# Kernel tuning notes

Hardware: AMD Instinct MI355X
Metric: run time of the kernel (lower is better)

The kernel has to match this reference:

```python
import jax, jax.numpy as jnp
import numpy as np

N = 1000        # genomes
S = 32          # samples
M = 2_000_000   # total genes
K = 100_000     # sequences (contigs)


def setup_inputs() -> dict:
    key = jax.random.key(0)
    k1, k2, k3, k4, k5 = jax.random.split(key, 5)
    A = jax.random.normal(k1, (N, S), dtype=jnp.float32)          # log-abundance
    B = jax.random.uniform(k2, (N, S), dtype=jnp.float32)         # log-PTR in [0,1]
    pos = jax.random.uniform(k3, (M,), dtype=jnp.float32)         # gene position in [0,1]
    genome_idx = jax.random.randint(k4, (M,), 0, N)               # one-hot column of `members`
    seq_idx = jax.random.randint(k5, (M,), 0, K)                  # row of `gene_to_seq`
    return {"A": A, "B": B, "pos": pos, "genome_idx": genome_idx, "seq_idx": seq_idx}


def reference(A, B, pos, genome_idx, seq_idx):
    # G = members @ A + 1 - dists @ B  ==  A[g] + 1 - pos * B[g] per gene  -> [M, S]
    G = A[genome_idx] + 1.0 - pos[:, None] * B[genome_idx]
    # E @ exp(G): sum exp(G) over genes belonging to each sequence -> [K, S]
    return jax.ops.segment_sum(jnp.exp(G), seq_idx, num_segments=K)
```

## Files before the change

kernel.cpp:

```cpp
#include <hip/hip_runtime.h>
#include <hip/hip_bf16.h>


#define CHUNK 8192
#define NBMAX 1024
#define CAPLG 12
#define CAP   (1 << CAPLG)

__device__ inline float fast_exp2(float x) {
    float r;
    asm("v_exp_f32 %0, %1" : "=v"(r) : "v"(x));
    return r;
}

__global__ __launch_bounds__(256) void prep_kernel(
    const float* __restrict__ A, const float* __restrict__ B,
    unsigned* __restrict__ AB2p, int* __restrict__ gcur, int NS)
{
    const int i = blockIdx.x * 256 + threadIdx.x;
    if (i < NBMAX) gcur[i] = 0;
    if (i >= NS) return;
    const float a2 = (A[i] + 1.0f) * 1.44269504f;
    const float b2 = B[i] * (1.44269504f / 32768.0f);
    const _Float16 ha = (_Float16)a2;
    const unsigned short ua = __builtin_bit_cast(unsigned short, ha);
    unsigned bb = __float_as_uint(b2);
    bb = (bb + 0x7FFFu + ((bb >> 16) & 1u)) & 0xFFFF0000u;
    AB2p[i] = (unsigned)ua | bb;
}

__global__ __launch_bounds__(1024) void partition_kernel(
    const float* __restrict__ pos, const int* __restrict__ gidx,
    const int* __restrict__ sidx, int* __restrict__ gcur,
    unsigned* __restrict__ payload, int M, int NB)
{
    __shared__ int h[NBMAX];
    __shared__ int pfx[NBMAX];
    __shared__ int cur[NBMAX];
    __shared__ int wsum[16];
    __shared__ unsigned stg_p[CHUNK];
    __shared__ unsigned short stg_b[CHUNK];
    const int t = threadIdx.x, blk = blockIdx.x;
    const int i0 = blk * CHUNK;
    const int n = min(CHUNK, M - i0);

    h[t] = 0;
    __syncthreads();
    for (int j = t; j < n; j += 1024) atomicAdd(&h[sidx[i0 + j] >> 7], 1);
    __syncthreads();

    {
        const int v = h[t];
        int incl = v;
#pragma unroll
        for (int d = 1; d < 64; d <<= 1) {
            const int x = __shfl_up(incl, d);
            if ((t & 63) >= d) incl += x;
        }
        if ((t & 63) == 63) wsum[t >> 6] = incl;
        __syncthreads();
        if (t < 16) {
            const int wv = wsum[t];
            int winc = wv;
#pragma unroll
            for (int d = 1; d < 16; d <<= 1) {
                const int x = __shfl_up(winc, d, 16);
                if (t >= d) winc += x;
            }
            wsum[t] = winc - wv;
        }
        __syncthreads();
        const int ex = wsum[t >> 6] + incl - v;
        pfx[t] = ex;
        cur[t] = ex;
    }
    __syncthreads();

    for (int j = t; j < n; j += 1024) {
        const int sx = sidx[i0 + j];
        const int b = sx >> 7;
        const float p = pos[i0 + j];
        int q = (int)fmaf(p, 32768.0f, 0.5f);
        q = min(q, 32767);
        const unsigned pl = (unsigned)(sx & 127)
                          | ((unsigned)gidx[i0 + j] << 7)
                          | ((unsigned)q << 17);
        const int d = atomicAdd(&cur[b], 1);
        stg_p[d] = pl;
        stg_b[d] = (unsigned short)b;
    }
    __syncthreads();

    if (t < NB) {
        const int hc = h[t];
        int dst = t << CAPLG;
        if (hc > 0) dst += atomicAdd(&gcur[t], hc);
        cur[t] = dst;
    }
    __syncthreads();

    for (int tt = t; tt < n; tt += 1024) {
        const int b = stg_b[tt];
        const int r = cur[b] + (tt - pfx[b]);
        if ((r >> CAPLG) == b) payload[r] = stg_p[tt];
    }
}

#define GENE(w, dst)                                                        \
    {                                                                       \
        const float qf = (float)((w) >> 17);                                \
        const unsigned ab = AB2p[(((w) >> 2) & 0x7FE0u) + s32];             \
        float a2v;                                                          \
        asm("v_cvt_f32_f16 %0, %1" : "=v"(a2v) : "v"(ab));                  \
        dst += fast_exp2(fmaf(-qf, __int_as_float(ab & 0xFFFF0000u), a2v)); \
    }

__global__ __launch_bounds__(512) void fused_reduce_kernel(
    const unsigned* __restrict__ AB2p, const unsigned* __restrict__ payload,
    const int* __restrict__ gcur, float* __restrict__ out, int K)
{
    __shared__ unsigned sorted[CAP];
    __shared__ int h[128];
    __shared__ int pfx[128];
    const int t = threadIdx.x, bkt = blockIdx.x;
    const int s32 = t & 31;
    const int half = (t >> 5) & 1;
    const int wv = t >> 6;
    const int start = bkt << CAPLG;
    const int n = min(gcur[bkt], CAP);

    if (t < 128) h[t] = 0;
    __syncthreads();

    unsigned r[8];
    int rk[8];
#pragma unroll
    for (int u = 0; u < 8; u++) {
        const int idx = t + u * 512;
        if (idx < n) {
            r[u] = payload[start + idx];
            rk[u] = atomicAdd(&h[r[u] & 127], 1);
        } else rk[u] = -1;
    }
    __syncthreads();

    if (t < 64) {
        const int e0 = h[2 * t], e1 = h[2 * t + 1];
        const int ps = e0 + e1;
        int incl = ps;
#pragma unroll
        for (int d = 1; d < 64; d <<= 1) {
            const int x = __shfl_up(incl, d);
            if (t >= d) incl += x;
        }
        const int ex = incl - ps;
        pfx[2 * t] = ex;
        pfx[2 * t + 1] = ex + e0;
    }
    __syncthreads();

#pragma unroll
    for (int u = 0; u < 8; u++)
        if (rk[u] >= 0) sorted[pfx[r[u] & 127] + rk[u]] = r[u];
    __syncthreads();

    const int seqbase = (bkt << 7) + (wv << 4);
    for (int q = 0; q < 16; q++) {
        const int ls = (wv << 4) + q;
        int i = pfx[ls];
        const int e = i + h[ls];
        float a0 = 0.0f, a1 = 0.0f;
        for (; i + 3 < e; i += 4) {
            const unsigned w0 = sorted[i + half];
            const unsigned w1 = sorted[i + 2 + half];
            GENE(w0, a0); GENE(w1, a1);
        }
        for (; i + 1 < e; i += 2) {
            const unsigned w0 = sorted[i + half];
            GENE(w0, a0);
        }
        if (i < e && half == 0) {
            const unsigned w0 = sorted[i];
            GENE(w0, a0);
        }
        float acc = a0 + a1;
        acc += __shfl_xor(acc, 32);
        const int seq = seqbase + q;
        if (half == 0 && seq < K) out[(seq << 5) + s32] = acc;
    }
}

__global__ __launch_bounds__(256) void scatter_exp_fallback(
    const float* __restrict__ A, const float* __restrict__ B,
    const float* __restrict__ pos, const int* __restrict__ gidx,
    const int* __restrict__ sidx, float* __restrict__ out, int M)
{
    const int lane = threadIdx.x & 31;
    int group = (int)((blockIdx.x * blockDim.x + threadIdx.x) >> 5);
    const int stride = (int)((gridDim.x * blockDim.x) >> 5);
    for (int g = group; g < M; g += stride) {
        const int gi = gidx[g];
        const int si = sidx[g];
        const float p = pos[g];
        const float a = A[(gi << 5) + lane];
        const float b = B[(gi << 5) + lane];
        atomicAdd(&out[(si << 5) + lane], __expf(fmaf(-p, b, a + 1.0f)));
    }
}

extern "C" void kernel_launch(void* const* d_in, const int* in_sizes, int n_in,
                              void* d_out, int out_size, void* d_ws, size_t ws_size,
                              hipStream_t stream)
{
    const float* A    = (const float*)d_in[0];
    const float* B    = (const float*)d_in[1];
    const float* pos  = (const float*)d_in[2];
    const int*   gidx = (const int*)d_in[3];
    const int*   sidx = (const int*)d_in[4];
    float*       out  = (float*)d_out;

    const int M  = in_sizes[2];
    const int NS = in_sizes[0];
    const int N  = NS / 32;
    const int K  = out_size / 32;
    const int NB = (K + 127) >> 7;
    const int NBLK = (M + CHUNK - 1) / CHUNK;

    char* ws = (char*)d_ws;
    size_t off = 0;
    int* gcur = (int*)(ws + off);       off += (size_t)NBMAX * sizeof(int);
    off = (off + 255) & ~(size_t)255;
    unsigned* AB2p = (unsigned*)(ws + off); off += (size_t)N * 32 * sizeof(unsigned);
    off = (off + 255) & ~(size_t)255;
    unsigned* payload = (unsigned*)(ws + off);
    const size_t need = off + ((size_t)NB << CAPLG) * sizeof(unsigned);

    const bool packable = (NB <= NBMAX) && (K <= NBMAX * 128) && (N <= 1024)
                       && (M / (NB > 0 ? NB : 1) <= CAP / 4 * 3);
    if (!packable || ws_size < need) {
        hipMemsetAsync(d_out, 0, (size_t)out_size * sizeof(float), stream);
        scatter_exp_fallback<<<8192, 256, 0, stream>>>(A, B, pos, gidx, sidx, out, M);
        return;
    }

    const int prep_grid = (max(NS, NBMAX) + 255) / 256;
    prep_kernel     <<<prep_grid, 256, 0, stream>>>(A, B, AB2p, gcur, NS);
    partition_kernel<<<NBLK, 1024, 0, stream>>>(pos, gidx, sidx, gcur, payload, M, NB);
    fused_reduce_kernel<<<NB, 512, 0, stream>>>(AB2p, payload, gcur, out, K);
}
```

Measured before the change: 65.99 us.

## Split each reduce bucket across two blocks and simplify gene address math

The fused reduce kernel now runs two blocks per 128-sequence bucket. Each block keeps only the entries whose sequence bit 6 matches its half, sorts them into a smaller 3072-entry shared buffer and reduces 64 sequences, which doubles the grid to raise occupancy and parallelism. The table lookup now builds a byte offset straight from the packed payload bits. Each half-wave also reads two adjacent sorted entries, so the shared-memory loads can be paired. In exchange every bucket's payload is read twice from global memory, and any half-bucket with more than 3072 entries would be silently truncated.

```diff
diff --git a/kernel.cpp b/kernel.cpp
--- a/kernel.cpp
+++ b/kernel.cpp
@@ -6,6 +6,7 @@
 #define NBMAX 1024
 #define CAPLG 12
 #define CAP   (1 << CAPLG)
+#define SCAP  3072
 
 __device__ inline float fast_exp2(float x) {
     float r;
@@ -109,7 +110,8 @@
 #define GENE(w, dst)                                                        \
     {                                                                       \
         const float qf = (float)((w) >> 17);                                \
-        const unsigned ab = AB2p[(((w) >> 2) & 0x7FE0u) + s32];             \
+        const unsigned voff = ((w) & 0x1FF80u) | lane4;                     \
+        const unsigned ab = *(const unsigned*)((const char*)AB2p + voff);   \
         float a2v;                                                          \
         asm("v_cvt_f32_f16 %0, %1" : "=v"(a2v) : "v"(ab));                  \
         dst += fast_exp2(fmaf(-qf, __int_as_float(ab & 0xFFFF0000u), a2v)); \
@@ -119,17 +121,20 @@
     const unsigned* __restrict__ AB2p, const unsigned* __restrict__ payload,
     const int* __restrict__ gcur, float* __restrict__ out, int K)
 {
-    __shared__ unsigned sorted[CAP];
-    __shared__ int h[128];
-    __shared__ int pfx[128];
-    const int t = threadIdx.x, bkt = blockIdx.x;
+    __shared__ unsigned sorted[SCAP];
+    __shared__ int h[64];
+    __shared__ int pfx[64];
+    const int t = threadIdx.x;
+    const int bkt = blockIdx.x >> 1;
+    const int sp  = blockIdx.x & 1;
     const int s32 = t & 31;
     const int half = (t >> 5) & 1;
     const int wv = t >> 6;
+    const unsigned lane4 = (unsigned)(s32 << 2);
     const int start = bkt << CAPLG;
     const int n = min(gcur[bkt], CAP);
 
-    if (t < 128) h[t] = 0;
+    if (t < 64) h[t] = 0;
     __syncthreads();
 
     unsigned r[8];
@@ -137,42 +142,47 @@
 #pragma unroll
     for (int u = 0; u < 8; u++) {
         const int idx = t + u * 512;
+        rk[u] = -1;
         if (idx < n) {
-            r[u] = payload[start + idx];
-            rk[u] = atomicAdd(&h[r[u] & 127], 1);
-        } else rk[u] = -1;
+            const unsigned w = payload[start + idx];
+            if ((int)((w >> 6) & 1u) == sp) {
+                r[u] = w;
+                rk[u] = atomicAdd(&h[w & 63], 1);
+            }
+        }
     }
     __syncthreads();
 
     if (t < 64) {
-        const int e0 = h[2 * t], e1 = h[2 * t + 1];
-        const int ps = e0 + e1;
-        int incl = ps;
+        const int v = h[t];
+        int incl = v;
 #pragma unroll
         for (int d = 1; d < 64; d <<= 1) {
             const int x = __shfl_up(incl, d);
             if (t >= d) incl += x;
         }
-        const int ex = incl - ps;
-        pfx[2 * t] = ex;
-        pfx[2 * t + 1] = ex + e0;
+        pfx[t] = incl - v;
     }
     __syncthreads();
 
 #pragma unroll
     for (int u = 0; u < 8; u++)
-        if (rk[u] >= 0) sorted[pfx[r[u] & 127] + rk[u]] = r[u];
-    __syncthreads();
-
-    const int seqbase = (bkt << 7) + (wv << 4);
-    for (int q = 0; q < 16; q++) {
-        const int ls = (wv << 4) + q;
+        if (rk[u] >= 0) {
+            const int d = pfx[r[u] & 63] + rk[u];
+            if (d < SCAP) sorted[d] = r[u];
+        }
+    __syncthreads();
+
+    const int seqbase = (bkt << 7) + (sp << 6) + (wv << 3);
+    for (int q = 0; q < 8; q++) {
+        const int ls = (wv << 3) + q;
         int i = pfx[ls];
-        const int e = i + h[ls];
+        const int e = min(i + h[ls], SCAP);
         float a0 = 0.0f, a1 = 0.0f;
         for (; i + 3 < e; i += 4) {
-            const unsigned w0 = sorted[i + half];
-            const unsigned w1 = sorted[i + 2 + half];
+            const int ix = i + (half << 1);
+            const unsigned w0 = sorted[ix];
+            const unsigned w1 = sorted[ix + 1];
             GENE(w0, a0); GENE(w1, a1);
         }
         for (; i + 1 < e; i += 2) {
@@ -246,5 +256,5 @@
     const int prep_grid = (max(NS, NBMAX) + 255) / 256;
     prep_kernel     <<<prep_grid, 256, 0, stream>>>(A, B, AB2p, gcur, NS);
     partition_kernel<<<NBLK, 1024, 0, stream>>>(pos, gidx, sidx, gcur, payload, M, NB);
-    fused_reduce_kernel<<<NB, 512, 0, stream>>>(AB2p, payload, gcur, out, K);
-}
+    fused_reduce_kernel<<<NB * 2, 512, 0, stream>>>(AB2p, payload, gcur, out, K);
+}
```

Measured after the change: 60.10 us. 8.9% less time.
